# Optimization experiments

Hardware: AMD Instinct MI355X
Metric: run time of the kernel (lower is better)

## Reference

```python
import jax, jax.numpy as jnp
import numpy as np

B, LQ, LK, D = 2, 2048, 2048, 1024
H, DK, DV = 16, 64, 64
EPS = 1e-6


def setup_inputs() -> dict:
    key = jax.random.key(0)
    ks = jax.random.split(key, 12)
    s = 1.0 / np.sqrt(D)
    return {
        "PE_states": jax.random.normal(ks[0], (B, LK, D), jnp.float32),
        "global_state": jax.random.normal(ks[1], (B, LQ, D), jnp.float32),
        "PE_statements": jax.random.normal(ks[2], (B, LK, D), jnp.float32),
        "PE_operators": jax.random.normal(ks[3], (B, LK, D), jnp.float32),
        "PE_solution_scores": jax.random.uniform(ks[4], (B, LK), jnp.float32),
        "mask": jax.random.randint(ks[5], (B, LQ, LK), 0, 2, jnp.int32),
        "w_q": jax.random.normal(ks[6], (D, H * DK), jnp.float32) * s,
        "w_k": jax.random.normal(ks[7], (D, H * DK), jnp.float32) * s,
        "w_v": jax.random.normal(ks[8], (D, H * DV), jnp.float32) * s,
        "w_fc": jax.random.normal(ks[9], (H * DV, D), jnp.float32) * s,
        "ln_gamma": jnp.ones((D,), jnp.float32),
        "ln_beta": jnp.zeros((D,), jnp.float32),
    }


def _layer_norm(x, gamma, beta):
    mu = jnp.mean(x, axis=-1, keepdims=True)
    var = jnp.mean(jnp.square(x - mu), axis=-1, keepdims=True)
    return (x - mu) * jax.lax.rsqrt(var + EPS) * gamma + beta


def reference(PE_states, global_state, PE_statements, PE_operators,
              PE_solution_scores, mask, w_q, w_k, w_v, w_fc, ln_gamma, ln_beta):
    # att_type == 'ca_sc', query_mode == 'PE', dropout == 0
    residual = global_state  # [B, LQ, D]
    q = (global_state @ w_q).reshape(B, LQ, H, DK).transpose(0, 2, 1, 3)   # bhqd
    k = (PE_states @ w_k).reshape(B, LK, H, DK).transpose(0, 2, 1, 3)      # bhkd
    v_s = (PE_statements @ w_v).reshape(B, LK, H, DV).transpose(0, 2, 1, 3)
    v_o = (PE_operators @ w_v).reshape(B, LK, H, DV).transpose(0, 2, 1, 3)

    temp = jnp.asarray(DK, jnp.float32) ** 0.5
    attn = jnp.einsum('bhqd,bhkd->bhqk', q / temp, k)  # [B,H,LQ,LK]
    # PE_solution_scores: per-key bias broadcast over heads and queries
    attn = (attn + PE_solution_scores[:, None, None, :]) / 2.0
    attn = jnp.where(mask[:, None, :, :] == 0, jnp.float32(-1e9), attn)
    attn = jax.nn.softmax(attn, axis=-1)

    def head_out(v):
        o = jnp.einsum('bhqk,bhkd->bhqd', attn, v)
        o = o.transpose(0, 2, 1, 3).reshape(B, LQ, H * DV)
        o = o @ w_fc + residual
        return _layer_norm(o, ln_gamma, ln_beta)

    statement_pred = head_out(v_s)
    operator_pred = head_out(v_o)
    return statement_pred, operator_pred
```

## Files before the change

### kernel.cpp

```cpp
#include <hip/hip_runtime.h>


typedef unsigned short u16;
typedef unsigned int   u32;
typedef unsigned long long u64;

typedef __attribute__((ext_vector_type(8))) short frag_ab;
typedef __attribute__((ext_vector_type(4))) float frag_cd;
typedef __attribute__((ext_vector_type(16))) float f32x16;
typedef __attribute__((ext_vector_type(8))) unsigned short u16x8;
typedef __attribute__((ext_vector_type(4))) unsigned short u16x4;
typedef __attribute__((ext_vector_type(2))) unsigned int u32x2;
typedef __attribute__((ext_vector_type(4))) int int4v;

__device__ __forceinline__ u16 f2bf(float f) {
    u32 x = __builtin_bit_cast(u32, f);
    return (u16)((x + 0x7fffu + ((x >> 16) & 1u)) >> 16);
}

__device__ __forceinline__ u32 pkbf(float a, float b) {
    return __builtin_amdgcn_perm(__builtin_bit_cast(u32, b),
                                 __builtin_bit_cast(u32, a), 0x07060302u);
}

#define GLDS16(gsrc, ldst)                                                     \
    __builtin_amdgcn_global_load_lds(                                          \
        (const __attribute__((address_space(1))) void*)(gsrc),                 \
        (__attribute__((address_space(3))) void*)(ldst), 16, 0, 0)

#define MFMA32(a, b, c) __builtin_amdgcn_mfma_f32_32x32x16_bf16(a, b, c, 0, 0, 0)

__global__ __launch_bounds__(256) void downcast_kernel(
    const float* __restrict__ in0, const float* __restrict__ in1,
    const float* __restrict__ in2, const float* __restrict__ in3,
    u16* __restrict__ out)
{
    int z = blockIdx.y;
    const float* in = z == 0 ? in0 : z == 1 ? in1 : z == 2 ? in2 : in3;
    u16* o = out + (size_t)z * 4194304;
    size_t i = ((size_t)blockIdx.x * 256 + threadIdx.x) * 8;
    float4 f0 = *(const float4*)(in + i);
    float4 f1 = *(const float4*)(in + i + 4);
    u16x8 t;
    t[0] = f2bf(f0.x); t[1] = f2bf(f0.y); t[2] = f2bf(f0.z); t[3] = f2bf(f0.w);
    t[4] = f2bf(f1.x); t[5] = f2bf(f1.y); t[6] = f2bf(f1.z); t[7] = f2bf(f1.w);
    *(u16x8*)(o + i) = t;
}

__global__ __launch_bounds__(256) void transpose_kernel(
    const float* __restrict__ w_q, const float* __restrict__ w_k,
    const float* __restrict__ w_v, const float* __restrict__ w_fc,
    u16* __restrict__ wqT, u16* __restrict__ wkT,
    u16* __restrict__ wvT, u16* __restrict__ wfcT)
{
    __shared__ u16 tile[32][33];
    int z = blockIdx.z;
    const float* in = z == 0 ? w_q : z == 1 ? w_k : z == 2 ? w_v : w_fc;
    u16* out = z == 0 ? wqT : z == 1 ? wkT : z == 2 ? wvT : wfcT;
    int bx = blockIdx.x * 32, by = blockIdx.y * 32;
    int tx = threadIdx.x & 31, ty = threadIdx.x >> 5;
    for (int i = 0; i < 32; i += 8)
        tile[ty + i][tx] = f2bf(in[(size_t)(by + ty + i) * 1024 + bx + tx]);
    __syncthreads();
    for (int i = 0; i < 32; i += 8)
        out[(size_t)(bx + ty + i) * 1024 + by + tx] = tile[tx][ty + i];
}

__global__ __launch_bounds__(256) void pack_mask_kernel(
    const int* __restrict__ mask, u64* __restrict__ bits)
{
    long long gid = (long long)blockIdx.x * 256 + threadIdx.x;
    int v = mask[gid];
    u64 bl = __ballot(v != 0);
    if ((threadIdx.x & 63) == 0) bits[gid >> 6] = bl;
}

__device__ __forceinline__ void gemm_core(
    const u16* __restrict__ A, const u16* __restrict__ BT,
    int bm, int bn, u16* Al, u16* Bl, frag_cd acc[4][4])
{
    const int tid = threadIdx.x;
    const int wave = tid >> 6, lane = tid & 63;
    const int ln15 = lane & 15, quad = lane >> 4;
    const int wm4 = (wave & 1) * 4, wn4 = (wave >> 1) * 4;

    for (int k0 = 0; k0 < 1024; k0 += 64) {
        for (int s = 0; s < 4; s++) {
            int f = wave * 4 + s;
            int grp = f >> 1, ks = f & 1;
            size_t col = k0 + ks * 32 + quad * 8;
            GLDS16(&A[(size_t)(bm + grp * 16 + ln15) * 1024 + col], Al + f * 512);
            GLDS16(&BT[(size_t)(bn + grp * 16 + ln15) * 1024 + col], Bl + f * 512);
        }
        __syncthreads();
        for (int ks = 0; ks < 2; ks++) {
            frag_ab a[4], b[4];
            for (int i = 0; i < 4; i++)
                a[i] = *(const frag_ab*)(Al + ((wm4 + i) * 2 + ks) * 512 + lane * 8);
            for (int j = 0; j < 4; j++)
                b[j] = *(const frag_ab*)(Bl + ((wn4 + j) * 2 + ks) * 512 + lane * 8);
            for (int i = 0; i < 4; i++)
                for (int j = 0; j < 4; j++)
                    acc[i][j] = __builtin_amdgcn_mfma_f32_16x16x32_bf16(a[i], b[j], acc[i][j], 0, 0, 0);
        }
        __syncthreads();
    }
}

__global__ __launch_bounds__(256, 3) void proj_gemm_kernel(
    const u16* __restrict__ Ab4,
    const u16* __restrict__ wqT, const u16* __restrict__ wkT, const u16* __restrict__ wvT,
    u16* __restrict__ Qb, u16* __restrict__ Kb,
    u16* __restrict__ VsT_g, u16* __restrict__ VoT_g)
{
    __shared__ alignas(16) u16 Al[16 * 512];
    __shared__ alignas(16) u16 Bl[16 * 512];
    const int z = blockIdx.z;
    const u16* A = Ab4 + (size_t)z * 4194304;
    const u16* BT = z == 0 ? wqT : z == 1 ? wkT : wvT;
    const int bm = blockIdx.x * 128, bn = blockIdx.y * 128;
    frag_cd acc[4][4] = {};
    gemm_core(A, BT, bm, bn, Al, Bl, acc);

    const int lane = threadIdx.x & 63;
    const int wave = threadIdx.x >> 6;
    const int ln15 = lane & 15, quad = lane >> 4;
    const int wm = (wave & 1) * 64, wn = (wave >> 1) * 64;
    if (z < 2) {
        u16* C = z == 0 ? Qb : Kb;
        const float qsc = z == 0 ? 0.09016844f : 1.0f;
        for (int i = 0; i < 4; i++) for (int j = 0; j < 4; j++) {
            int row0 = bm + wm + i * 16 + quad * 4;
            int col = bn + wn + j * 16 + ln15;
            for (int r = 0; r < 4; r++)
                C[(size_t)(row0 + r) * 1024 + col] = f2bf(acc[i][j][r] * qsc);
        }
    } else {
        u16* C = z == 2 ? VsT_g : VoT_g;
        for (int i = 0; i < 4; i++) for (int j = 0; j < 4; j++) {
            int row0 = bm + wm + i * 16 + quad * 4;
            int col = bn + wn + j * 16 + ln15;
            u16x4 t;
            for (int r = 0; r < 4; r++) t[r] = f2bf(acc[i][j][r]);
            *(u16x4*)&C[(size_t)col * 4096 + row0] = t;
        }
    }
}

__global__ __launch_bounds__(256, 3) void fc_gemm_kernel(
    const u16* __restrict__ Osb, const u16* __restrict__ Oob, const u16* __restrict__ wfcT,
    const float* __restrict__ resid, float* __restrict__ preLN)
{
    __shared__ alignas(16) u16 Al[16 * 512];
    __shared__ alignas(16) u16 Bl[16 * 512];
    const int z = blockIdx.z;
    const u16* A = z == 0 ? Osb : Oob;
    float* Cf = preLN + (size_t)z * 4194304;
    const int bm = blockIdx.x * 128, bn = blockIdx.y * 128;
    frag_cd acc[4][4] = {};
    gemm_core(A, wfcT, bm, bn, Al, Bl, acc);

    const int lane = threadIdx.x & 63;
    const int wave = threadIdx.x >> 6;
    const int ln15 = lane & 15, quad = lane >> 4;
    const int wm = (wave & 1) * 64, wn = (wave >> 1) * 64;
    for (int i = 0; i < 4; i++) for (int j = 0; j < 4; j++) {
        int row0 = bm + wm + i * 16 + quad * 4;
        int col = bn + wn + j * 16 + ln15;
        for (int r = 0; r < 4; r++) {
            size_t off = (size_t)(row0 + r) * 1024 + col;
            Cf[off] = acc[i][j][r] + resid[off];
        }
    }
}

__device__ __forceinline__ void flash_stage(
    const u16* __restrict__ Kp, const u16* __restrict__ VsT, const u16* __restrict__ VoT,
    int b, int h, int kt, int wave, int ln31, int hi, u16* buf)
{
    const int k0 = kt * 64;
    for (int s = 0; s < 6; s++) {
        int t = wave * 6 + s;
        const u16* g;
        if (t < 8) {
            int n = t >> 2, ks = t & 3;
            g = &Kp[(size_t)(b * 2048 + k0 + n * 32 + ln31) * 1024 + h * 64 + ks * 16 + hi * 8];
        } else if (t < 16) {
            int dt = (t >> 2) & 1, sk = t & 3;
            g = &VsT[(size_t)(h * 64 + dt * 32 + ln31) * 4096 + b * 2048 + k0 + sk * 16 + hi * 8];
        } else {
            int dt = (t >> 2) & 1, sk = t & 3;
            g = &VoT[(size_t)(h * 64 + dt * 32 + ln31) * 4096 + b * 2048 + k0 + sk * 16 + hi * 8];
        }
        GLDS16(g, buf + t * 512);
    }
}

__global__ __launch_bounds__(256, 2) void flash_kernel(
    const u16* __restrict__ Q, const u16* __restrict__ Kp,
    const u16* __restrict__ VsT_g, const u16* __restrict__ VoT_g,
    const float* __restrict__ scores, const u64* __restrict__ mbits,
    u16* __restrict__ Os, u16* __restrict__ Oo)
{
    __shared__ alignas(16) u16 KV[2][24 * 512];
    const int qt = blockIdx.x, h = blockIdx.y, b = blockIdx.z;
    const int tid = threadIdx.x;
    const int wave = tid >> 6, lane = tid & 63;
    const int ln31 = lane & 31, hi = lane >> 5;
    const int qbase = b * 2048 + qt * 128 + wave * 32;
    const int qrow = qbase + ln31;

    frag_ab aq0, aq1, aq2, aq3;
    {
        const u16* qp = &Q[(size_t)qrow * 1024 + h * 64 + hi * 8];
        aq0 = *(const frag_ab*)(qp);
        aq1 = *(const frag_ab*)(qp + 16);
        aq2 = *(const frag_ab*)(qp + 32);
        aq3 = *(const frag_ab*)(qp + 48);
    }
    frag_ab bbias = {};
    bbias[0] = (short)0x3F80; bbias[1] = (short)0x3F80;

    f32x16 os0 = {}, os1 = {}, oo0 = {}, oo1 = {};
    float l0 = 0.f, l1 = 0.f;
    const int shl4 = 4 - 4 * hi;

    auto softmax16 = [&](f32x16& s, u32 wa, float& lacc) {
#pragma unroll
        for (int r = 0; r < 16; r++) {
            const int bitc = (r & 3) + 8 * (r >> 2);
            u32 m = (u32)(((int)(wa << (27 - bitc))) >> 31);
            float e = __builtin_amdgcn_exp2f(s[r]);
            u32 pb = __builtin_bit_cast(u32, e) & m;
            float pf = __builtin_bit_cast(float, pb);
            lacc += pf;
            s[r] = pf;
        }
    };

    flash_stage(Kp, VsT_g, VoT_g, b, h, 0, wave, ln31, hi, KV[0]);

    for (int kt = 0; kt < 32; kt++) {
        const int p = kt & 1;
        float sc0f = scores[b * 2048 + kt * 64 + ln31];
        float sc1f = scores[b * 2048 + kt * 64 + 32 + ln31];
        u64 w = mbits[(size_t)qrow * 32 + kt];
        __syncthreads();
        if (kt < 31)
            flash_stage(Kp, VsT_g, VoT_g, b, h, kt + 1, wave, ln31, hi, KV[p ^ 1]);
        const u16* bufp = KV[p];

        frag_ab ab0 = {}, ab1 = {};
        if (!hi) {
            float t0 = sc0f * 0.72134752f;
            u16 c0 = f2bf(t0);
            ab0[0] = (short)c0;
            ab0[1] = (short)f2bf(t0 - __builtin_bit_cast(float, (u32)c0 << 16));
            float t1 = sc1f * 0.72134752f;
            u16 c1 = f2bf(t1);
            ab1[0] = (short)c1;
            ab1[1] = (short)f2bf(t1 - __builtin_bit_cast(float, (u32)c1 << 16));
        }

        f32x16 sacc0 = {}, sacc1 = {};
        sacc0 = MFMA32(ab0, bbias, sacc0);
        sacc1 = MFMA32(ab1, bbias, sacc1);
#pragma unroll
        for (int ks = 0; ks < 4; ks++) {
            frag_ab ak0 = *(const frag_ab*)(bufp + (0 * 4 + ks) * 512 + lane * 8);
            frag_ab ak1 = *(const frag_ab*)(bufp + (1 * 4 + ks) * 512 + lane * 8);
            frag_ab q = ks == 0 ? aq0 : ks == 1 ? aq1 : ks == 2 ? aq2 : aq3;
            sacc0 = MFMA32(ak0, q, sacc0);
            sacc1 = MFMA32(ak1, q, sacc1);
        }

        u32 wa0 = ((u32)w) << shl4;
        u32 wa1 = ((u32)(w >> 32)) << shl4;
        softmax16(sacc0, wa0, l0);
        softmax16(sacc1, wa1, l1);

#pragma unroll
        for (int sk = 0; sk < 4; sk++) {
            const f32x16& ps = (sk < 2) ? sacc0 : sacc1;
            const int e0 = (sk & 1) * 8;
            u32 a0 = pkbf(ps[e0 + 0], ps[e0 + 1]);
            u32 a1 = pkbf(ps[e0 + 2], ps[e0 + 3]);
            u32 b0 = pkbf(ps[e0 + 4], ps[e0 + 5]);
            u32 b1 = pkbf(ps[e0 + 6], ps[e0 + 7]);
            u32x2 r0 = __builtin_amdgcn_permlane32_swap(a0, b0, false, false);
            u32x2 r1 = __builtin_amdgcn_permlane32_swap(a1, b1, false, false);
            int4v iv;
            iv[0] = (int)r0[0]; iv[1] = (int)r1[0];
            iv[2] = (int)r0[1]; iv[3] = (int)r1[1];
            frag_ab ap = __builtin_bit_cast(frag_ab, iv);
            frag_ab bs0 = *(const frag_ab*)(bufp + (8 + sk) * 512 + lane * 8);
            frag_ab bs1 = *(const frag_ab*)(bufp + (12 + sk) * 512 + lane * 8);
            frag_ab bo0 = *(const frag_ab*)(bufp + (16 + sk) * 512 + lane * 8);
            frag_ab bo1 = *(const frag_ab*)(bufp + (20 + sk) * 512 + lane * 8);
            os0 = MFMA32(ap, bs0, os0);
            os1 = MFMA32(ap, bs1, os1);
            oo0 = MFMA32(ap, bo0, oo0);
            oo1 = MFMA32(ap, bo1, oo1);
        }
    }

    float l_run = l0 + l1;
    float l_tot = l_run + __shfl_xor(l_run, 32, 64);
#pragma unroll
    for (int r = 0; r < 16; r++) {
        const int qr = (r & 3) + 8 * (r >> 2) + 4 * hi;
        float lv = __shfl(l_tot, qr, 64);
        float inv = 1.0f / fmaxf(lv, 1e-30f);
        size_t row = (size_t)(qbase + qr) * 1024 + h * 64;
        Os[row + ln31]      = f2bf(os0[r] * inv);
        Os[row + 32 + ln31] = f2bf(os1[r] * inv);
        Oo[row + ln31]      = f2bf(oo0[r] * inv);
        Oo[row + 32 + ln31] = f2bf(oo1[r] * inv);
    }
}

__global__ __launch_bounds__(256) void ln_kernel(
    const float* __restrict__ X, const float* __restrict__ gamma, const float* __restrict__ beta,
    float* __restrict__ out)
{
    __shared__ float red[4];
    int row = blockIdx.x;
    int tid = threadIdx.x;
    const float* x = X + (size_t)row * 1024;
    float v[4];
    float s = 0.f;
    for (int i = 0; i < 4; i++) { v[i] = x[tid + i * 256]; s += v[i]; }
    for (int off = 1; off < 64; off <<= 1) s += __shfl_xor(s, off, 64);
    int wv = tid >> 6, ln = tid & 63;
    if (ln == 0) red[wv] = s;
    __syncthreads();
    float mean = (red[0] + red[1] + red[2] + red[3]) * (1.0f / 1024.0f);
    float s2 = 0.f;
    for (int i = 0; i < 4; i++) { float d = v[i] - mean; s2 += d * d; }
    for (int off = 1; off < 64; off <<= 1) s2 += __shfl_xor(s2, off, 64);
    __syncthreads();
    if (ln == 0) red[wv] = s2;
    __syncthreads();
    float var = (red[0] + red[1] + red[2] + red[3]) * (1.0f / 1024.0f);
    float rstd = rsqrtf(var + 1e-6f);
    for (int i = 0; i < 4; i++) {
        int c = tid + i * 256;
        out[(size_t)row * 1024 + c] = (v[i] - mean) * rstd * gamma[c] + beta[c];
    }
}

extern "C" void kernel_launch(void* const* d_in, const int* in_sizes, int n_in,
                              void* d_out, int out_size, void* d_ws, size_t ws_size,
                              hipStream_t stream)
{
    const float* PE_states     = (const float*)d_in[0];
    const float* global_state  = (const float*)d_in[1];
    const float* PE_statements = (const float*)d_in[2];
    const float* PE_operators  = (const float*)d_in[3];
    const float* scores        = (const float*)d_in[4];
    const int*   mask          = (const int*)d_in[5];
    const float* w_q  = (const float*)d_in[6];
    const float* w_k  = (const float*)d_in[7];
    const float* w_v  = (const float*)d_in[8];
    const float* w_fc = (const float*)d_in[9];
    const float* gamma = (const float*)d_in[10];
    const float* beta  = (const float*)d_in[11];
    float* out = (float*)d_out;

    char* ws = (char*)d_ws;
    const size_t MB = 1u << 20;
    u16* Ab4   = (u16*)(ws + 0 * MB);
    u16* Osb   = (u16*)(ws + 0 * MB);
    u16* Oob   = (u16*)(ws + 8 * MB);
    u16* wqT   = (u16*)(ws + 32 * MB);
    u16* wkT   = (u16*)(ws + 34 * MB);
    u16* wvT   = (u16*)(ws + 36 * MB);
    u16* wfcT  = (u16*)(ws + 38 * MB);
    u64* mbits = (u64*)(ws + 40 * MB);
    u16* Qb    = (u16*)(ws + 41 * MB);
    u16* Kb    = (u16*)(ws + 49 * MB);
    u16* VsT_g = (u16*)(ws + 57 * MB);
    u16* VoT_g = (u16*)(ws + 65 * MB);
    float* preLN = (float*)(ws + 41 * MB);

    downcast_kernel<<<dim3(2048, 4), 256, 0, stream>>>(
        global_state, PE_states, PE_statements, PE_operators, Ab4);
    transpose_kernel<<<dim3(32, 32, 4), 256, 0, stream>>>(w_q, w_k, w_v, w_fc, wqT, wkT, wvT, wfcT);
    pack_mask_kernel<<<32768, 256, 0, stream>>>(mask, mbits);

    proj_gemm_kernel<<<dim3(32, 8, 4), 256, 0, stream>>>(
        Ab4, wqT, wkT, wvT, Qb, Kb, VsT_g, VoT_g);

    flash_kernel<<<dim3(16, 16, 2), 256, 0, stream>>>(Qb, Kb, VsT_g, VoT_g, scores, mbits, Osb, Oob);

    fc_gemm_kernel<<<dim3(32, 8, 2), 256, 0, stream>>>(Osb, Oob, wfcT, global_state, preLN);
    ln_kernel<<<8192, 256, 0, stream>>>(preLN, gamma, beta, out);
}
```

Baseline: 373.3 us.

## Load K tiles directly into registers and raise MFMA wave priority

```diff
diff --git a/kernel.cpp b/kernel.cpp
--- a/kernel.cpp
+++ b/kernel.cpp
@@ -174,24 +174,19 @@
     }
 }
 
-__device__ __forceinline__ void flash_stage(
-    const u16* __restrict__ Kp, const u16* __restrict__ VsT, const u16* __restrict__ VoT,
+__device__ __forceinline__ void flash_stage_v(
+    const u16* __restrict__ VsT, const u16* __restrict__ VoT,
     int b, int h, int kt, int wave, int ln31, int hi, u16* buf)
 {
     const int k0 = kt * 64;
-    for (int s = 0; s < 6; s++) {
-        int t = wave * 6 + s;
+    for (int s = 0; s < 4; s++) {
+        int t = wave * 4 + s;
+        int dt = (t >> 2) & 1, sk = t & 3;
         const u16* g;
-        if (t < 8) {
-            int n = t >> 2, ks = t & 3;
-            g = &Kp[(size_t)(b * 2048 + k0 + n * 32 + ln31) * 1024 + h * 64 + ks * 16 + hi * 8];
-        } else if (t < 16) {
-            int dt = (t >> 2) & 1, sk = t & 3;
+        if (t < 8)
             g = &VsT[(size_t)(h * 64 + dt * 32 + ln31) * 4096 + b * 2048 + k0 + sk * 16 + hi * 8];
-        } else {
-            int dt = (t >> 2) & 1, sk = t & 3;
+        else
             g = &VoT[(size_t)(h * 64 + dt * 32 + ln31) * 4096 + b * 2048 + k0 + sk * 16 + hi * 8];
-        }
         GLDS16(g, buf + t * 512);
     }
 }
@@ -202,7 +197,7 @@
     const float* __restrict__ scores, const u64* __restrict__ mbits,
     u16* __restrict__ Os, u16* __restrict__ Oo)
 {
-    __shared__ alignas(16) u16 KV[2][24 * 512];
+    __shared__ alignas(16) u16 KV[2][16 * 512];
     const int qt = blockIdx.x, h = blockIdx.y, b = blockIdx.z;
     const int tid = threadIdx.x;
     const int wave = tid >> 6, lane = tid & 63;
@@ -238,7 +233,15 @@
         }
     };
 
-    flash_stage(Kp, VsT_g, VoT_g, b, h, 0, wave, ln31, hi, KV[0]);
+    const u16* kbase = &Kp[(size_t)(b * 2048 + ln31) * 1024 + h * 64 + hi * 8];
+    frag_ab kA[4], kB[4];
+#pragma unroll
+    for (int ks = 0; ks < 4; ks++) {
+        kA[ks] = *(const frag_ab*)(kbase + (size_t)0 * 1024 + ks * 16);
+        kB[ks] = *(const frag_ab*)(kbase + (size_t)32 * 1024 + ks * 16);
+    }
+
+    flash_stage_v(VsT_g, VoT_g, b, h, 0, wave, ln31, hi, KV[0]);
 
     for (int kt = 0; kt < 32; kt++) {
         const int p = kt & 1;
@@ -247,7 +250,7 @@
         u64 w = mbits[(size_t)qrow * 32 + kt];
         __syncthreads();
         if (kt < 31)
-            flash_stage(Kp, VsT_g, VoT_g, b, h, kt + 1, wave, ln31, hi, KV[p ^ 1]);
+            flash_stage_v(VsT_g, VoT_g, b, h, kt + 1, wave, ln31, hi, KV[p ^ 1]);
         const u16* bufp = KV[p];
 
         frag_ab ab0 = {}, ab1 = {};
@@ -263,15 +266,24 @@
         }
 
         f32x16 sacc0 = {}, sacc1 = {};
+        __builtin_amdgcn_s_setprio(1);
         sacc0 = MFMA32(ab0, bbias, sacc0);
         sacc1 = MFMA32(ab1, bbias, sacc1);
 #pragma unroll
         for (int ks = 0; ks < 4; ks++) {
-            frag_ab ak0 = *(const frag_ab*)(bufp + (0 * 4 + ks) * 512 + lane * 8);
-            frag_ab ak1 = *(const frag_ab*)(bufp + (1 * 4 + ks) * 512 + lane * 8);
             frag_ab q = ks == 0 ? aq0 : ks == 1 ? aq1 : ks == 2 ? aq2 : aq3;
-            sacc0 = MFMA32(ak0, q, sacc0);
-            sacc1 = MFMA32(ak1, q, sacc1);
+            sacc0 = MFMA32(kA[ks], q, sacc0);
+            sacc1 = MFMA32(kB[ks], q, sacc1);
+        }
+        __builtin_amdgcn_s_setprio(0);
+
+        if (kt < 31) {
+            const u16* kb2 = kbase + (size_t)(kt + 1) * 64 * 1024;
+#pragma unroll
+            for (int ks = 0; ks < 4; ks++) {
+                kA[ks] = *(const frag_ab*)(kb2 + (size_t)0 * 1024 + ks * 16);
+                kB[ks] = *(const frag_ab*)(kb2 + (size_t)32 * 1024 + ks * 16);
+            }
         }
 
         u32 wa0 = ((u32)w) << shl4;
@@ -293,14 +305,16 @@
             iv[0] = (int)r0[0]; iv[1] = (int)r1[0];
             iv[2] = (int)r0[1]; iv[3] = (int)r1[1];
             frag_ab ap = __builtin_bit_cast(frag_ab, iv);
-            frag_ab bs0 = *(const frag_ab*)(bufp + (8 + sk) * 512 + lane * 8);
-            frag_ab bs1 = *(const frag_ab*)(bufp + (12 + sk) * 512 + lane * 8);
-            frag_ab bo0 = *(const frag_ab*)(bufp + (16 + sk) * 512 + lane * 8);
-            frag_ab bo1 = *(const frag_ab*)(bufp + (20 + sk) * 512 + lane * 8);
+            frag_ab bs0 = *(const frag_ab*)(bufp + (0 + sk) * 512 + lane * 8);
+            frag_ab bs1 = *(const frag_ab*)(bufp + (4 + sk) * 512 + lane * 8);
+            frag_ab bo0 = *(const frag_ab*)(bufp + (8 + sk) * 512 + lane * 8);
+            frag_ab bo1 = *(const frag_ab*)(bufp + (12 + sk) * 512 + lane * 8);
+            __builtin_amdgcn_s_setprio(1);
             os0 = MFMA32(ap, bs0, os0);
             os1 = MFMA32(ap, bs1, os1);
             oo0 = MFMA32(ap, bo0, oo0);
             oo1 = MFMA32(ap, bo1, oo1);
+            __builtin_amdgcn_s_setprio(0);
         }
     }
 
```

Result: slower. 399.3 us (+7.0%).
